# Performance work log

Measured on AMD Instinct MI355X. Metric: run time of the kernel, lower is better.

The kernel has to match this reference:

```python
import jax, jax.numpy as jnp
import numpy as np

# ---- static config (matches init_kwargs) ----
N_NODES = 100_000; N_GRAPHS = 100; NPG = 1000; GRID = 32  # ceil(sqrt(1000))
N_EDGES = 1_600_000
IN_DIM = 64; POS_DIM = 16; HID = 16; HEADS = 4; HD = HID * HEADS  # 64
OUT_DIM = 10; DIV_WEIGHT = 0.1; BN_EPS = 1e-5; NEG_SLOPE = 0.2


def _segment_softmax(e, dst, n):
    emax = jax.ops.segment_max(e, dst, num_segments=n)
    p = jnp.exp(e - emax[dst])
    denom = jax.ops.segment_sum(p, dst, num_segments=n)
    return p / (denom[dst] + 1e-16)


def _gat(x, src, dst, n, W, a_src, a_dst, extra=None):
    """GATv1-style conv: per-head linear, additive attention, segment softmax over dst."""
    H, D = a_src.shape
    h = (x @ W).reshape(n, H, D)          # [N,H,D]
    s = (h * a_src).sum(-1)               # [N,H]
    d = (h * a_dst).sum(-1)               # [N,H]
    e = s[src] + d[dst]
    if extra is not None:
        e = e + extra                     # positional attention bias [E,H]
    e = jax.nn.leaky_relu(e, NEG_SLOPE)
    alpha = _segment_softmax(e, dst, n)   # [E,H]
    out = jax.ops.segment_sum(alpha[:, :, None] * h[src], dst, num_segments=n)
    return out.reshape(n, H * D)


def _div_loss(W):
    # head-diversity / orthogonality regularizer on per-head weight slices
    in_dim = W.shape[0]
    Wh = W.reshape(in_dim, HEADS, HID).transpose(1, 0, 2).reshape(HEADS, -1)
    Wn = Wh / (jnp.linalg.norm(Wh, axis=-1, keepdims=True) + 1e-12)
    G = Wn @ Wn.T
    off = G - jnp.eye(HEADS, dtype=W.dtype)
    return DIV_WEIGHT * (off ** 2).sum() / (HEADS * (HEADS - 1))


def _grid_pos(n, dtype):
    # normalized grid positions per graph (equal-size graphs of NPG nodes)
    i = jnp.arange(n) % NPG
    return jnp.stack([(i // GRID) / (GRID - 1), (i % GRID) / (GRID - 1)], -1).astype(dtype)


def _forward(x, edge_index, batch,
             pe_W, pe_b,
             l0_pW, l0_pas, l0_pad, l0_posW, l0_posb, l0_dW, l0_das, l0_dad, l0_fW, l0_fb, l0_g, l0_b,
             l1_pW, l1_pas, l1_pad, l1_posW, l1_posb, l1_dW, l1_das, l1_dad, l1_fW, l1_fb, l1_g, l1_b,
             res_W, res_b, task_W, task_b):
    n = x.shape[0]
    src, dst = edge_index[0], edge_index[1]
    pos = _grid_pos(n, x.dtype)
    rel = pos[dst] - pos[src]             # [E,2]
    h = jnp.concatenate([x, pos @ pe_W + pe_b], -1)  # positional encoding concat [N,80]

    def layer(h_in, pW, pas, pad, posW, posb, dW, das, dad, fW, fb, g, b):
        pos_out = _gat(h_in, src, dst, n, pW, pas, pad, extra=rel @ posW + posb)
        div_out = _gat(h_in, src, dst, n, dW, das, dad)
        fused = jnp.concatenate([pos_out, div_out], -1) @ fW + fb
        mu = fused.mean(0)
        var = fused.var(0)
        bn = (fused - mu) / jnp.sqrt(var + BN_EPS) * g + b
        return jax.nn.elu(bn), _div_loss(dW)

    h1, dl0 = layer(h, l0_pW, l0_pas, l0_pad, l0_posW, l0_posb, l0_dW, l0_das, l0_dad, l0_fW, l0_fb, l0_g, l0_b)
    h2, dl1 = layer(h1, l1_pW, l1_pas, l1_pad, l1_posW, l1_posb, l1_dW, l1_das, l1_dad, l1_fW, l1_fb, l1_g, l1_b)
    h2 = h2 + (h1 @ res_W + res_b)        # residual on layer >0

    pooled = jax.ops.segment_sum(h2, batch, num_segments=N_GRAPHS) / NPG  # mean pool
    task = pooled @ task_W + task_b       # [N_GRAPHS, OUT_DIM]
    return task, dl0 + dl1


def setup_inputs() -> dict:
    key = jax.random.key(0)
    keys = iter(jax.random.split(key, 64))
    nk = lambda: next(keys)
    w = lambda shape: jax.random.normal(nk(), shape, jnp.float32) * 0.05
    x = jax.random.normal(nk(), (N_NODES, IN_DIM), jnp.float32)
    gid = jnp.repeat(jnp.arange(N_GRAPHS), N_EDGES // N_GRAPHS)
    src = gid * NPG + jax.random.randint(nk(), (N_EDGES,), 0, NPG)
    dst = gid * NPG + jax.random.randint(nk(), (N_EDGES,), 0, NPG)
    edge_index = jnp.stack([src, dst]).astype(jnp.int32)
    batch = jnp.repeat(jnp.arange(N_GRAPHS), NPG).astype(jnp.int32)
    IN0 = IN_DIM + POS_DIM
    inp = dict(x=x, edge_index=edge_index, batch=batch,
               pe_W=w((2, POS_DIM)), pe_b=jnp.zeros((POS_DIM,), jnp.float32))
    for pref, din in (('l0', IN0), ('l1', HD)):
        inp[pref + '_pW'] = w((din, HD)); inp[pref + '_pas'] = w((HEADS, HID)); inp[pref + '_pad'] = w((HEADS, HID))
        inp[pref + '_posW'] = w((2, HEADS)); inp[pref + '_posb'] = jnp.zeros((HEADS,), jnp.float32)
        inp[pref + '_dW'] = w((din, HD)); inp[pref + '_das'] = w((HEADS, HID)); inp[pref + '_dad'] = w((HEADS, HID))
        inp[pref + '_fW'] = w((2 * HD, HD)); inp[pref + '_fb'] = jnp.zeros((HD,), jnp.float32)
        inp[pref + '_g'] = jnp.ones((HD,), jnp.float32); inp[pref + '_b'] = jnp.zeros((HD,), jnp.float32)
    inp['res_W'] = w((HD, HD)); inp['res_b'] = jnp.zeros((HD,), jnp.float32)
    inp['task_W'] = w((HD, OUT_DIM)); inp['task_b'] = jnp.zeros((OUT_DIM,), jnp.float32)
    return inp


def reference(x, edge_index, batch,
              pe_W, pe_b,
              l0_pW, l0_pas, l0_pad, l0_posW, l0_posb, l0_dW, l0_das, l0_dad, l0_fW, l0_fb, l0_g, l0_b,
              l1_pW, l1_pas, l1_pad, l1_posW, l1_posb, l1_dW, l1_das, l1_dad, l1_fW, l1_fb, l1_g, l1_b,
              res_W, res_b, task_W, task_b):
    return _forward(x, edge_index, batch, pe_W, pe_b,
                    l0_pW, l0_pas, l0_pad, l0_posW, l0_posb, l0_dW, l0_das, l0_dad, l0_fW, l0_fb, l0_g, l0_b,
                    l1_pW, l1_pas, l1_pad, l1_posW, l1_posb, l1_dW, l1_das, l1_dad, l1_fW, l1_fb, l1_g, l1_b,
                    res_W, res_b, task_W, task_b)
```

## Files before the change

kernel.cpp:

```cpp
#include <hip/hip_runtime.h>
#include <math.h>

#define N_NODES   100000
#define N_GRAPHS  100
#define NPG       1000
#define N_EDGES   1600000
#define EPG       16000
#define HID       16
#define HEADS     4
#define HD        64
#define OUT_DIM   10
#define BN_EPS    1e-5f
#define NEG_SLOPE 0.2f

#define LDA 68
#define GG_BLOCKS 6250

static const size_t OFF_SPART = 0;
static const size_t OFF_PEWS  = 7000000;
static const size_t OFF_STAT1 = 7001000;
static const size_t OFF_WFRAG = 7010000;
static const size_t OFF_WF2   = 7020000;
static const size_t OFF_POOL  = 7100000;
static const size_t OFF_HL    = 8000000;
static const size_t OFF_F0    = 33600000;
static const size_t OFF_F1    = 40000000;
static const size_t OFF_SPSP  = 46400000;
static const size_t OFF_SPSD  = 46800000;
static const size_t OFF_DPD   = 47200000;
static const size_t OFF_STATS = 48000000;
static const size_t OFF_CSR   = 48000128;
static const size_t OFF_SRT   = 48100144;

__device__ inline unsigned bf_pack(float x, float y) {
    unsigned ux = __float_as_uint(x);
    unsigned uy = __float_as_uint(y);
    ux = (ux + 0x7FFFu + ((ux >> 16) & 1u)) >> 16;
    uy = ((uy + 0x7FFFu + ((uy >> 16) & 1u)) >> 16) << 16;
    return ux | uy;
}
__device__ inline float bf_lo(unsigned u) { return __uint_as_float(u << 16); }
__device__ inline float bf_hi(unsigned u) { return __uint_as_float(u & 0xFFFF0000u); }

typedef __attribute__((ext_vector_type(8))) short bf16x8;
typedef __attribute__((ext_vector_type(4))) float f32x4;

__device__ inline bf16x8 frag_from(unsigned a, unsigned b, unsigned c, unsigned d) {
    uint4 u{a, b, c, d};
    return *reinterpret_cast<bf16x8*>(&u);
}

__global__ __launch_bounds__(1024) void sort_edges(const int* __restrict__ ei,
                                                   int* __restrict__ csr_off,
                                                   int* __restrict__ sorted_src) {
    __shared__ int hist[1024];
    __shared__ int scan[1024];
    const int g = blockIdx.x;
    const int t = threadIdx.x;
    const int* src = ei;
    const int* dst = ei + N_EDGES;
    const int e0 = g * EPG;
    const int nbase = g * NPG;

    hist[t] = 0;
    __syncthreads();
    for (int i = t; i < EPG; i += 1024) {
        int d = dst[e0 + i] - nbase;
        atomicAdd(&hist[d], 1);
    }
    __syncthreads();
    scan[t] = hist[t];
    __syncthreads();
    for (int off = 1; off < 1024; off <<= 1) {
        int v = (t >= off) ? scan[t - off] : 0;
        __syncthreads();
        scan[t] += v;
        __syncthreads();
    }
    int excl = scan[t] - hist[t];
    if (t < NPG) csr_off[nbase + t] = e0 + excl;
    if (g == 0 && t == 0) csr_off[N_NODES] = N_EDGES;
    __syncthreads();
    hist[t] = excl;
    __syncthreads();
    for (int i = t; i < EPG; i += 1024) {
        int s = src[e0 + i];
        int d = dst[e0 + i] - nbase;
        int slot = atomicAdd(&hist[d], 1);
        sorted_src[e0 + slot] = s;
    }
}

__global__ __launch_bounds__(256) void prep_all(const float* __restrict__ peW, const float* __restrict__ peb,
                                                const float* __restrict__ pW0, const float* __restrict__ dW0,
                                                const float* __restrict__ pW1, const float* __restrict__ dW1,
                                                const float* __restrict__ fW0, const float* __restrict__ fW1,
                                                float* __restrict__ pe,
                                                uint4* __restrict__ wfA,
                                                uint4* __restrict__ wfD,
                                                float* __restrict__ pool2,
                                                float* __restrict__ stats0,
                                                float* __restrict__ stats1) {
    const int t = threadIdx.x;
    const int b = blockIdx.x;
    if (b == 0) {
        if (t < 128) {
            int r = t >> 6, c = t & 63;
            float sp = 0.f, sd = 0.f;
            for (int m = 0; m < 16; ++m) {
                sp += peW[r * 16 + m] * pW0[(64 + m) * 64 + c];
                sd += peW[r * 16 + m] * dW0[(64 + m) * 64 + c];
            }
            pe[r * 64 + c] = sp;
            pe[192 + r * 64 + c] = sd;
        } else if (t < 192) {
            int c = t & 63;
            float sp = 0.f, sd = 0.f;
            for (int m = 0; m < 16; ++m) {
                sp += peb[m] * pW0[(64 + m) * 64 + c];
                sd += peb[m] * dW0[(64 + m) * 64 + c];
            }
            pe[128 + c] = sp;
            pe[320 + c] = sd;
        }
    } else if (b == 1) {
        for (int i = t; i < 2 * 4 * 4 * 64; i += 256) {
            const int lane  = i & 63;
            const int ct    = (i >> 6) & 3;
            const int kk    = (i >> 8) & 3;
            const int layer = i >> 10;
            const float* W = layer ? fW1 : fW0;
            const int col = ct * 16 + (lane & 15);
            const int kb  = kk * 32 + (lane >> 4) * 8;
            uint4 u;
            u.x = bf_pack(W[(kb + 0) * 64 + col], W[(kb + 1) * 64 + col]);
            u.y = bf_pack(W[(kb + 2) * 64 + col], W[(kb + 3) * 64 + col]);
            u.z = bf_pack(W[(kb + 4) * 64 + col], W[(kb + 5) * 64 + col]);
            u.w = bf_pack(W[(kb + 6) * 64 + col], W[(kb + 7) * 64 + col]);
            wfA[i] = u;
        }
    } else if (b == 2) {
        for (int i = t; i < 2048; i += 256) {
            const int lane  = i & 63;
            const int ct    = (i >> 6) & 3;
            const int kk    = (i >> 8) & 1;
            const int mat   = (i >> 9) & 1;
            const int layer = i >> 10;
            const float* W = layer ? (mat ? dW1 : pW1) : (mat ? dW0 : pW0);
            const int col = ct * 16 + (lane & 15);
            const int kb  = kk * 32 + (lane >> 4) * 8;
            uint4 u;
            u.x = bf_pack(W[(kb + 0) * 64 + col], W[(kb + 1) * 64 + col]);
            u.y = bf_pack(W[(kb + 2) * 64 + col], W[(kb + 3) * 64 + col]);
            u.z = bf_pack(W[(kb + 4) * 64 + col], W[(kb + 5) * 64 + col]);
            u.w = bf_pack(W[(kb + 6) * 64 + col], W[(kb + 7) * 64 + col]);
            wfD[i] = u;
        }
    } else {
        for (int i = t; i < 2 * N_GRAPHS * 64; i += 256) pool2[i] = 0.f;
        if (t < 128) { stats0[t] = 0.f; stats1[t] = 0.f; }
    }
}

__global__ __launch_bounds__(128) void reduce_stats(const float* __restrict__ part,
                                                    float* __restrict__ stats, int nb) {
    const int c = threadIdx.x;
    const int per = (nb + gridDim.x - 1) / gridDim.x;
    const int b0 = blockIdx.x * per;
    int b1 = b0 + per; if (b1 > nb) b1 = nb;
    float s = 0.f;
    for (int b = b0; b < b1; ++b) s += part[(size_t)b * 128 + c];
    atomicAdd(&stats[c], s);
}

template <bool PE, bool BN>
__global__ __launch_bounds__(256) void gemm_dual_mfma(const float* __restrict__ A,
                                                      const unsigned* __restrict__ wf2,
                                                      const float* __restrict__ pe,
                                                      const float* __restrict__ pas,
                                                      const float* __restrict__ pad_,
                                                      const float* __restrict__ das,
                                                      const float* __restrict__ dad,
                                                      const float* __restrict__ posW,
                                                      const float* __restrict__ posb,
                                                      const float* __restrict__ stats,
                                                      const float* __restrict__ gamma,
                                                      const float* __restrict__ beta,
                                                      float* __restrict__ poolF,
                                                      unsigned* __restrict__ hl,
                                                      float* __restrict__ sps_p,
                                                      float* __restrict__ sps_d,
                                                      float2* __restrict__ dpd) {
    __shared__ float sD[4 * 2 * 16 * LDA];
    const int t = threadIdx.x;
    const int w = t >> 6, lane = t & 63;
    const int cidx = lane & 15, khi = lane >> 4;
    const int node0 = blockIdx.x * 64;

    bf16x8 wf[2][2][4];
#pragma unroll
    for (int mat = 0; mat < 2; ++mat)
#pragma unroll
        for (int kk = 0; kk < 2; ++kk)
#pragma unroll
            for (int ct = 0; ct < 4; ++ct)
                wf[mat][kk][ct] = *reinterpret_cast<const bf16x8*>(
                    wf2 + (size_t)((((mat * 2 + kk) * 4 + ct) * 64) + lane) * 4);

    const int node0w = node0 + w * 16;
    int gn = node0w + cidx; if (gn > N_NODES - 1) gn = N_NODES - 1;
    const float* ar = A + (size_t)gn * 64;
    bf16x8 ah[2], al[2];
#pragma unroll
    for (int kk = 0; kk < 2; ++kk) {
        const int k0 = kk * 32 + khi * 8;
        float4 f0 = *reinterpret_cast<const float4*>(ar + k0);
        float4 f1 = *reinterpret_cast<const float4*>(ar + k0 + 4);
        if (BN) {
            const float invN = 1.0f / (float)N_NODES;
            float4 sa = *reinterpret_cast<const float4*>(&stats[k0]);
            float4 sb = *reinterpret_cast<const float4*>(&stats[k0 + 4]);
            float4 qa = *reinterpret_cast<const float4*>(&stats[64 + k0]);
            float4 qb = *reinterpret_cast<const float4*>(&stats[64 + k0 + 4]);
            float4 ga = *reinterpret_cast<const float4*>(&gamma[k0]);
            float4 gb = *reinterpret_cast<const float4*>(&gamma[k0 + 4]);
            float4 ba = *reinterpret_cast<const float4*>(&beta[k0]);
            float4 bb = *reinterpret_cast<const float4*>(&beta[k0 + 4]);
            float sc[8], sh[8];
            float ss[8] = {sa.x, sa.y, sa.z, sa.w, sb.x, sb.y, sb.z, sb.w};
            float qq[8] = {qa.x, qa.y, qa.z, qa.w, qb.x, qb.y, qb.z, qb.w};
            float gg[8] = {ga.x, ga.y, ga.z, ga.w, gb.x, gb.y, gb.z, gb.w};
            float bt[8] = {ba.x, ba.y, ba.z, ba.w, bb.x, bb.y, bb.z, bb.w};
#pragma unroll
            for (int i = 0; i < 8; ++i) {
                float mu = ss[i] * invN;
                float var = qq[i] * invN - mu * mu;
                float iv = rsqrtf(var + BN_EPS);
                sc[i] = iv * gg[i];
                sh[i] = bt[i] - mu * sc[i];
            }
            auto ap = [&](float v, int i) {
                float r = fmaf(v, sc[i], sh[i]);
                return r > 0.f ? r : (__expf(r) - 1.f);
            };
            f0.x = ap(f0.x, 0); f0.y = ap(f0.y, 1); f0.z = ap(f0.z, 2); f0.w = ap(f0.w, 3);
            f1.x = ap(f1.x, 4); f1.y = ap(f1.y, 5); f1.z = ap(f1.z, 6); f1.w = ap(f1.w, 7);
            if (node0w < N_NODES) {
                const int node_l = node0w + cidx;
                const bool okn = node_l < N_NODES;
                const int gl = node_l / NPG;
                const int g0 = node0w / NPG;
                int lastn = node0w + 15; if (lastn > N_NODES - 1) lastn = N_NODES - 1;
                const int g1 = lastn / NPG;
                float p8[8] = {f0.x, f0.y, f0.z, f0.w, f1.x, f1.y, f1.z, f1.w};
                {
                    const bool m = okn && (gl == g0);
#pragma unroll
                    for (int i = 0; i < 8; ++i) {
                        float tv = m ? p8[i] : 0.f;
                        tv += __shfl_xor(tv, 1); tv += __shfl_xor(tv, 2);
                        tv += __shfl_xor(tv, 4); tv += __shfl_xor(tv, 8);
                        if (cidx == 0) atomicAdd(&poolF[g0 * 64 + k0 + i], tv);
                    }
                }
                if (g1 != g0) {
                    const bool m = okn && (gl == g1);
#pragma unroll
                    for (int i = 0; i < 8; ++i) {
                        float tv = m ? p8[i] : 0.f;
                        tv += __shfl_xor(tv, 1); tv += __shfl_xor(tv, 2);
                        tv += __shfl_xor(tv, 4); tv += __shfl_xor(tv, 8);
                        if (cidx == 0) atomicAdd(&poolF[g1 * 64 + k0 + i], tv);
                    }
                }
            }
        }
        unsigned h0 = bf_pack(f0.x, f0.y), h1 = bf_pack(f0.z, f0.w);
        unsigned h2 = bf_pack(f1.x, f1.y), h3 = bf_pack(f1.z, f1.w);
        unsigned l0 = bf_pack(f0.x - bf_lo(h0), f0.y - bf_hi(h0));
        unsigned l1 = bf_pack(f0.z - bf_lo(h1), f0.w - bf_hi(h1));
        unsigned l2 = bf_pack(f1.x - bf_lo(h2), f1.y - bf_hi(h2));
        unsigned l3 = bf_pack(f1.z - bf_lo(h3), f1.w - bf_hi(h3));
        ah[kk] = frag_from(h0, h1, h2, h3);
        al[kk] = frag_from(l0, l1, l2, l3);
    }

    f32x4 ap4[4], ad4[4];
#pragma unroll
    for (int ct = 0; ct < 4; ++ct) { ap4[ct] = 0.f; ad4[ct] = 0.f; }
#pragma unroll
    for (int ct = 0; ct < 4; ++ct) {
        ap4[ct] = __builtin_amdgcn_mfma_f32_16x16x32_bf16(ah[0], wf[0][0][ct], ap4[ct], 0, 0, 0);
        ap4[ct] = __builtin_amdgcn_mfma_f32_16x16x32_bf16(ah[1], wf[0][1][ct], ap4[ct], 0, 0, 0);
        ap4[ct] = __builtin_amdgcn_mfma_f32_16x16x32_bf16(al[0], wf[0][0][ct], ap4[ct], 0, 0, 0);
        ap4[ct] = __builtin_amdgcn_mfma_f32_16x16x32_bf16(al[1], wf[0][1][ct], ap4[ct], 0, 0, 0);
        ad4[ct] = __builtin_amdgcn_mfma_f32_16x16x32_bf16(ah[0], wf[1][0][ct], ad4[ct], 0, 0, 0);
        ad4[ct] = __builtin_amdgcn_mfma_f32_16x16x32_bf16(ah[1], wf[1][1][ct], ad4[ct], 0, 0, 0);
        ad4[ct] = __builtin_amdgcn_mfma_f32_16x16x32_bf16(al[0], wf[1][0][ct], ad4[ct], 0, 0, 0);
        ad4[ct] = __builtin_amdgcn_mfma_f32_16x16x32_bf16(al[1], wf[1][1][ct], ad4[ct], 0, 0, 0);
    }

    {
        float* base = sD + w * (2 * 16 * LDA);
#pragma unroll
        for (int ct = 0; ct < 4; ++ct)
#pragma unroll
            for (int q = 0; q < 4; ++q) {
                base[(khi * 4 + q) * LDA + ct * 16 + cidx]                 = ap4[ct][q];
                base[16 * LDA + (khi * 4 + q) * LDA + ct * 16 + cidx]      = ad4[ct][q];
            }
    }
    __syncthreads();

    const int tx = t & 15, ty = t >> 4;
    const int c4 = tx * 4;
    float4 accp[4], accd[4];
#pragma unroll
    for (int j = 0; j < 4; ++j) {
        const int n = ty * 4 + j;
        const float* bp = sD + (n >> 4) * (2 * 16 * LDA) + (n & 15) * LDA;
        accp[j] = *reinterpret_cast<const float4*>(bp + c4);
        accd[j] = *reinterpret_cast<const float4*>(bp + 16 * LDA + c4);
    }

    if (PE) {
        float4 pp0 = *reinterpret_cast<const float4*>(&pe[c4]);
        float4 pp1 = *reinterpret_cast<const float4*>(&pe[64 + c4]);
        float4 ppb = *reinterpret_cast<const float4*>(&pe[128 + c4]);
        float4 pd0 = *reinterpret_cast<const float4*>(&pe[192 + c4]);
        float4 pd1 = *reinterpret_cast<const float4*>(&pe[256 + c4]);
        float4 pdb = *reinterpret_cast<const float4*>(&pe[320 + c4]);
#pragma unroll
        for (int j = 0; j < 4; ++j) {
            int node = node0 + ty * 4 + j;
            int r = node % NPG;
            float px = (float)(r >> 5) * (1.0f / 31.0f);
            float py = (float)(r & 31) * (1.0f / 31.0f);
            accp[j].x += px * pp0.x + py * pp1.x + ppb.x;
            accp[j].y += px * pp0.y + py * pp1.y + ppb.y;
            accp[j].z += px * pp0.z + py * pp1.z + ppb.z;
            accp[j].w += px * pp0.w + py * pp1.w + ppb.w;
            accd[j].x += px * pd0.x + py * pd1.x + pdb.x;
            accd[j].y += px * pd0.y + py * pd1.y + pdb.y;
            accd[j].z += px * pd0.z + py * pd1.z + pdb.z;
            accd[j].w += px * pd0.w + py * pd1.w + pdb.w;
        }
    }

    float4 pasv = *reinterpret_cast<const float4*>(&pas[c4]);
    float4 padv = *reinterpret_cast<const float4*>(&pad_[c4]);
    float4 dasv = *reinterpret_cast<const float4*>(&das[c4]);
    float4 dadv = *reinterpret_cast<const float4*>(&dad[c4]);
    const int h = tx >> 2;
    const float pw0 = posW[h], pw1 = posW[4 + h], pb = posb[h];
    const int cu = tx * 2;
#pragma unroll
    for (int j = 0; j < 4; ++j) {
        const int node = node0 + ty * 4 + j;
        float vps = accp[j].x * pasv.x + accp[j].y * pasv.y + accp[j].z * pasv.z + accp[j].w * pasv.w;
        float vpd = accp[j].x * padv.x + accp[j].y * padv.y + accp[j].z * padv.z + accp[j].w * padv.w;
        float vds = accd[j].x * dasv.x + accd[j].y * dasv.y + accd[j].z * dasv.z + accd[j].w * dasv.w;
        float vdd = accd[j].x * dadv.x + accd[j].y * dadv.y + accd[j].z * dadv.z + accd[j].w * dadv.w;
        vps += __shfl_xor(vps, 1); vps += __shfl_xor(vps, 2);
        vpd += __shfl_xor(vpd, 1); vpd += __shfl_xor(vpd, 2);
        vds += __shfl_xor(vds, 1); vds += __shfl_xor(vds, 2);
        vdd += __shfl_xor(vdd, 1); vdd += __shfl_xor(vdd, 2);
        if (node < N_NODES) {
            uint2 up, ud;
            up.x = bf_pack(accp[j].x, accp[j].y); up.y = bf_pack(accp[j].z, accp[j].w);
            ud.x = bf_pack(accd[j].x, accd[j].y); ud.y = bf_pack(accd[j].z, accd[j].w);
            *reinterpret_cast<uint2*>(&hl[(size_t)node * 64 + cu])      = up;
            *reinterpret_cast<uint2*>(&hl[(size_t)node * 64 + 32 + cu]) = ud;
            if ((tx & 3) == 0) {
                const int r = node % NPG;
                const float pxn = (float)(r >> 5) * (1.0f / 31.0f);
                const float pyn = (float)(r & 31) * (1.0f / 31.0f);
                const float posdot = pxn * pw0 + pyn * pw1;
                sps_p[node * 4 + h] = vps - posdot;
                sps_d[node * 4 + h] = vds;
                dpd[node * 4 + h] = float2{vpd + posdot + pb, vdd};
            }
        }
    }
}

__global__ __launch_bounds__(256) void gat_gemm(const unsigned* __restrict__ hl,
                                                const float* __restrict__ sps_p,
                                                const float* __restrict__ sps_d,
                                                const float2* __restrict__ dpd,
                                                const int* __restrict__ csr_off,
                                                const int* __restrict__ sorted_src,
                                                const unsigned* __restrict__ wfrag,
                                                const float* __restrict__ bias,
                                                float* __restrict__ outF,
                                                float* __restrict__ spart) {
    __shared__ unsigned sCat[16 * LDA];
    const int t = threadIdx.x;
    const int w = t >> 6, lane = t & 63;

    const int orig = blockIdx.x;
    const int xcd = orig & 7;
    const int qq = GG_BLOCKS >> 3, rr = GG_BLOCKS & 7;
    const int lb = (xcd < rr ? xcd * (qq + 1) : rr * (qq + 1) + (xcd - rr) * qq) + (orig >> 3);
    const int node0 = lb * 16;

    const int j1 = lane >> 3;
    const int p1 = (lane >> 2) & 1;
    const int h1 = lane & 3;
    const int phneed = ((lane >> 5) << 2) | ((lane & 31) >> 3);
    const float* __restrict__ spl = p1 ? sps_d : sps_p;

    for (int i = 0; i < 4; ++i) {
        const int v = node0 + w * 4 + i;
        const float2 dv1 = dpd[(size_t)v * 4 + h1];
        const float dval1 = p1 ? dv1.y : dv1.x;
        const int beg = __builtin_amdgcn_readfirstlane(csr_off[v]);
        const int end = __builtin_amdgcn_readfirstlane(csr_off[v + 1]);

        float2 acc = {0.f, 0.f};
        float wpart = 0.f;
        int e = beg;
        const int nfull = (end - beg) >> 3;

        int sA = 0, sB = 0;
        float svA = 0.f, svB = 0.f;
        if (nfull >= 1) { sA = sorted_src[e + j1]; svA = spl[(size_t)sA * 4 + h1]; }
        if (nfull >= 2) { sB = sorted_src[e + 8 + j1]; }

        for (int k = 0; k < nfull; ++k, e += 8) {
            int sC = 0;
            if (k + 2 < nfull) sC = sorted_src[e + 16 + j1];
            if (k + 1 < nfull) svB = spl[(size_t)sB * 4 + h1];
            float elog = svA + dval1;
            elog = fmaxf(elog, NEG_SLOPE * elog);
            float wv = __expf(elog);
            wpart += wv;
#pragma unroll
            for (int jj = 0; jj < 8; ++jj) {
                int sj = __builtin_amdgcn_readlane(sA, jj * 8);
                float wj = __shfl(wv, jj * 8 + phneed);
                unsigned u = hl[((size_t)sj << 6) + lane];
                acc.x = fmaf(wj, bf_lo(u), acc.x);
                acc.y = fmaf(wj, bf_hi(u), acc.y);
            }
            sA = sB; sB = sC; svA = svB;
        }

        if (e < end) {
            const int nj = end - e;
            int ee = e + j1; if (ee >= end) ee = end - 1;
            int s = sorted_src[ee];
            float sval = spl[(size_t)s * 4 + h1];
            float elog = sval + dval1;
            elog = fmaxf(elog, NEG_SLOPE * elog);
            float wv = __expf(elog);
            if (j1 >= nj) wv = 0.f;
            wpart += wv;
            for (int jj = 0; jj < nj; ++jj) {
                int sj = __builtin_amdgcn_readlane(s, jj * 8);
                float wj = __shfl(wv, jj * 8 + phneed);
                unsigned u = hl[((size_t)sj << 6) + lane];
                acc.x = fmaf(wj, bf_lo(u), acc.x);
                acc.y = fmaf(wj, bf_hi(u), acc.y);
            }
        }
        wpart += __shfl_xor(wpart, 8);
        wpart += __shfl_xor(wpart, 16);
        wpart += __shfl_xor(wpart, 32);
        const float wsum = __shfl(wpart, phneed);
        const float inv = 1.0f / (wsum + 1e-16f);
        sCat[(w * 4 + i) * LDA + lane] = bf_pack(acc.x * inv, acc.y * inv);
    }
    __syncthreads();

    const int cidx = lane & 15, khi = lane >> 4;
    bf16x8 wfr[4];
#pragma unroll
    for (int kk = 0; kk < 4; ++kk)
        wfr[kk] = *reinterpret_cast<const bf16x8*>(wfrag + (size_t)((kk * 4 + w) * 64 + lane) * 4);
    const float biasv = bias[w * 16 + cidx];

    f32x4 acc4 = 0.f;
#pragma unroll
    for (int kk = 0; kk < 4; ++kk) {
        bf16x8 a = *reinterpret_cast<const bf16x8*>(&sCat[cidx * LDA + kk * 16 + khi * 4]);
        acc4 = __builtin_amdgcn_mfma_f32_16x16x32_bf16(a, wfr[kk], acc4, 0, 0, 0);
    }

    float ls = 0.f, lq = 0.f;
#pragma unroll
    for (int q = 0; q < 4; ++q) {
        float v = acc4[q] + biasv;
        outF[(size_t)(node0 + khi * 4 + q) * 64 + w * 16 + cidx] = v;
        ls += v;
        lq = fmaf(v, v, lq);
    }
    ls += __shfl_xor(ls, 16); ls += __shfl_xor(ls, 32);
    lq += __shfl_xor(lq, 16); lq += __shfl_xor(lq, 32);
    if (khi == 0) {
        spart[(size_t)lb * 128 + w * 16 + cidx]      = ls;
        spart[(size_t)lb * 128 + 64 + w * 16 + cidx] = lq;
    }
}

template <bool WRITEF>
__global__ __launch_bounds__(256) void bn_elu(float* __restrict__ F, const float* __restrict__ stats,
                                              const float* __restrict__ gamma, const float* __restrict__ beta,
                                              float* __restrict__ pooled) {
    __shared__ float red[256];
    const int t = threadIdx.x;
    const int idx = blockIdx.x * 256 + t;
    const int c = t & 63;
    float mu = stats[c] * (1.0f / (float)N_NODES);
    float var = stats[64 + c] * (1.0f / (float)N_NODES) - mu * mu;
    float inv = rsqrtf(var + BN_EPS);
    float v = (F[idx] - mu) * inv * gamma[c] + beta[c];
    v = (v > 0.f) ? v : expm1f(v);
    if (WRITEF) F[idx] = v;
    red[t] = v;
    __syncthreads();
    if (t < 64) {
        float s = red[c] + red[64 + c] + red[128 + c] + red[192 + c];
        int g = (blockIdx.x * 4) / NPG;
        atomicAdd(&pooled[g * 64 + c], s);
    }
}

__global__ __launch_bounds__(64) void task_head(const float* __restrict__ pooled,
                                                const float* __restrict__ pooledF0,
                                                const float* __restrict__ resW,
                                                const float* __restrict__ resb,
                                                const float* __restrict__ taskW,
                                                const float* __restrict__ taskb,
                                                float* __restrict__ out) {
    const int g = blockIdx.x;
    const int c = threadIdx.x;
    float rc = 0.f;
    const float* pf = pooledF0 + g * 64;
    for (int k = 0; k < 64; ++k)
        rc = fmaf(pf[k], resW[k * 64 + c], rc);
    float p = (pooled[g * 64 + c] + rc) * (1.0f / (float)NPG) + resb[c];
#pragma unroll
    for (int o = 0; o < OUT_DIM; ++o) {
        float partial = p * taskW[c * OUT_DIM + o];
#pragma unroll
        for (int m = 1; m < 64; m <<= 1) partial += __shfl_xor(partial, m);
        if (c == 0) out[g * OUT_DIM + o] = partial + taskb[o];
    }
}

__global__ __launch_bounds__(256) void div_loss(const float* __restrict__ dW0,
                                                const float* __restrict__ dW1,
                                                float* __restrict__ out) {
    __shared__ float red[16][16];
    float total = 0.f;
    for (int layer = 0; layer < 2; ++layer) {
        const float* W = layer ? dW1 : dW0;
        const int din = layer ? 64 : 80;
        const int p = threadIdx.x & 15;
        const int s16 = threadIdx.x >> 4;
        const int i = p >> 2, j = p & 3;
        float acc = 0.f;
        const int Kk = din * 16;
        for (int kk = s16; kk < Kk; kk += 16) {
            int rrow = kk >> 4, cc = kk & 15;
            acc += W[rrow * 64 + i * 16 + cc] * W[rrow * 64 + j * 16 + cc];
        }
        red[p][s16] = acc;
        __syncthreads();
        if (threadIdx.x < 16) {
            float s = 0.f;
            for (int m = 0; m < 16; ++m) s += red[threadIdx.x][m];
            red[threadIdx.x][0] = s;
        }
        __syncthreads();
        if (threadIdx.x == 0) {
            float G[4][4], nrm[4];
            for (int a = 0; a < 4; ++a)
                for (int b = 0; b < 4; ++b) G[a][b] = red[a * 4 + b][0];
            for (int a = 0; a < 4; ++a) nrm[a] = sqrtf(G[a][a]) + 1e-12f;
            float l = 0.f;
            for (int a = 0; a < 4; ++a)
                for (int b = 0; b < 4; ++b) {
                    float gn = G[a][b] / (nrm[a] * nrm[b]);
                    float off = gn - (a == b ? 1.f : 0.f);
                    l += off * off;
                }
            total += 0.1f * l / 12.f;
        }
        __syncthreads();
    }
    if (threadIdx.x == 0) *out = total;
}

extern "C" void kernel_launch(void* const* d_in, const int* in_sizes, int n_in,
                              void* d_out, int out_size, void* d_ws, size_t ws_size,
                              hipStream_t stream) {
    const float* x      = (const float*)d_in[0];
    const int*   ei     = (const int*)d_in[1];
    const float* peW    = (const float*)d_in[3];
    const float* peb    = (const float*)d_in[4];

    const float* l_pW[2]   = {(const float*)d_in[5],  (const float*)d_in[17]};
    const float* l_pas[2]  = {(const float*)d_in[6],  (const float*)d_in[18]};
    const float* l_pad[2]  = {(const float*)d_in[7],  (const float*)d_in[19]};
    const float* l_posW[2] = {(const float*)d_in[8],  (const float*)d_in[20]};
    const float* l_posb[2] = {(const float*)d_in[9],  (const float*)d_in[21]};
    const float* l_dW[2]   = {(const float*)d_in[10], (const float*)d_in[22]};
    const float* l_das[2]  = {(const float*)d_in[11], (const float*)d_in[23]};
    const float* l_dad[2]  = {(const float*)d_in[12], (const float*)d_in[24]};
    const float* l_fW[2]   = {(const float*)d_in[13], (const float*)d_in[25]};
    const float* l_fb[2]   = {(const float*)d_in[14], (const float*)d_in[26]};
    const float* l_g[2]    = {(const float*)d_in[15], (const float*)d_in[27]};
    const float* l_b[2]    = {(const float*)d_in[16], (const float*)d_in[28]};
    const float* res_W  = (const float*)d_in[29];
    const float* res_b  = (const float*)d_in[30];
    const float* task_W = (const float*)d_in[31];
    const float* task_b = (const float*)d_in[32];

    float* ws = (float*)d_ws;
    float* spart   = ws + OFF_SPART;
    float* pe_ws   = ws + OFF_PEWS;
    float* stats1  = ws + OFF_STAT1;
    float* wfrag   = ws + OFF_WFRAG;
    float* wfrag2  = ws + OFF_WF2;
    float* pooled  = ws + OFF_POOL;
    float* pooledF0= ws + OFF_POOL + 6400;
    unsigned* hl   = (unsigned*)(ws + OFF_HL);
    float* F0      = ws + OFF_F0;
    float* F1      = ws + OFF_F1;
    float* sps_p   = ws + OFF_SPSP;
    float* sps_d   = ws + OFF_SPSD;
    float2* dpd    = (float2*)(ws + OFF_DPD);
    float* stats0  = ws + OFF_STATS;
    int*   csr_off    = (int*)(ws + OFF_CSR);
    int*   sorted_src = (int*)(ws + OFF_SRT);
    float* out = (float*)d_out;

    const int GEMM_BLOCKS = (N_NODES + 63) / 64;
    const int BN_BLOCKS   = N_NODES * 64 / 256;

    sort_edges<<<N_GRAPHS, 1024, 0, stream>>>(ei, csr_off, sorted_src);
    prep_all<<<4, 256, 0, stream>>>(peW, peb, l_pW[0], l_dW[0], l_pW[1], l_dW[1],
                                    l_fW[0], l_fW[1], pe_ws,
                                    (uint4*)wfrag, (uint4*)wfrag2,
                                    pooled, stats0, stats1);

    gemm_dual_mfma<true, false><<<GEMM_BLOCKS, 256, 0, stream>>>(x, (const unsigned*)wfrag2, pe_ws,
        l_pas[0], l_pad[0], l_das[0], l_dad[0], l_posW[0], l_posb[0],
        stats0, l_g[0], l_b[0], pooledF0,
        hl, sps_p, sps_d, dpd);
    gat_gemm<<<GG_BLOCKS, 256, 0, stream>>>(hl, sps_p, sps_d, dpd, csr_off, sorted_src,
        (const unsigned*)wfrag, l_fb[0], F0, spart);
    reduce_stats<<<32, 128, 0, stream>>>(spart, stats0, GG_BLOCKS);

    gemm_dual_mfma<false, true><<<GEMM_BLOCKS, 256, 0, stream>>>(F0, (const unsigned*)wfrag2 + 4096, pe_ws,
        l_pas[1], l_pad[1], l_das[1], l_dad[1], l_posW[1], l_posb[1],
        stats0, l_g[0], l_b[0], pooledF0,
        hl, sps_p, sps_d, dpd);
    gat_gemm<<<GG_BLOCKS, 256, 0, stream>>>(hl, sps_p, sps_d, dpd, csr_off, sorted_src,
        (const unsigned*)wfrag + 4096, l_fb[1], F1, spart);
    reduce_stats<<<32, 128, 0, stream>>>(spart, stats1, GG_BLOCKS);
    bn_elu<false><<<BN_BLOCKS, 256, 0, stream>>>(F1, stats1, l_g[1], l_b[1], pooled);

    task_head<<<N_GRAPHS, 64, 0, stream>>>(pooled, pooledF0, res_W, res_b,
                                           task_W, task_b, out);
    div_loss<<<1, 256, 0, stream>>>(l_dW[0], l_dW[1], out + 1000);
}
```

Before: 501.1 us.

## Merge sort and prep kernels, batch gather loads, coarsen final BN-pool

Folds the weight-prep kernel into the edge-sort launch as extra blocks, which removes one kernel launch. Rewrites the gather inner loop so all eight neighbor row loads are issued before any FMA, aiming for more memory-level parallelism. Replaces the per-element bn_elu with a pool_bn kernel where each block handles 200 nodes. This cuts the block count and the pooled atomics sharply, at the cost of far fewer blocks in flight.

```diff
diff --git a/kernel.cpp b/kernel.cpp
--- a/kernel.cpp
+++ b/kernel.cpp
@@ -15,6 +15,8 @@
 
 #define LDA 68
 #define GG_BLOCKS 6250
+#define PB_PER_GRAPH 5
+#define PB_NODES 200
 
 static const size_t OFF_SPART = 0;
 static const size_t OFF_PEWS  = 7000000;
@@ -50,13 +52,87 @@
     return *reinterpret_cast<bf16x8*>(&u);
 }
 
-__global__ __launch_bounds__(1024) void sort_edges(const int* __restrict__ ei,
-                                                   int* __restrict__ csr_off,
-                                                   int* __restrict__ sorted_src) {
+__global__ __launch_bounds__(1024) void sort_prep(const int* __restrict__ ei,
+                                                  int* __restrict__ csr_off,
+                                                  int* __restrict__ sorted_src,
+                                                  const float* __restrict__ peW, const float* __restrict__ peb,
+                                                  const float* __restrict__ pW0, const float* __restrict__ dW0,
+                                                  const float* __restrict__ pW1, const float* __restrict__ dW1,
+                                                  const float* __restrict__ fW0, const float* __restrict__ fW1,
+                                                  float* __restrict__ pe,
+                                                  uint4* __restrict__ wfA,
+                                                  uint4* __restrict__ wfD,
+                                                  float* __restrict__ pool2,
+                                                  float* __restrict__ stats0,
+                                                  float* __restrict__ stats1) {
+    const int g = blockIdx.x;
+    const int t = threadIdx.x;
+    if (g >= N_GRAPHS) {
+        const int b = g - N_GRAPHS;
+        if (b == 0) {
+            if (t < 128) {
+                int r = t >> 6, c = t & 63;
+                float sp = 0.f, sd = 0.f;
+                for (int m = 0; m < 16; ++m) {
+                    sp += peW[r * 16 + m] * pW0[(64 + m) * 64 + c];
+                    sd += peW[r * 16 + m] * dW0[(64 + m) * 64 + c];
+                }
+                pe[r * 64 + c] = sp;
+                pe[192 + r * 64 + c] = sd;
+            } else if (t < 192) {
+                int c = t & 63;
+                float sp = 0.f, sd = 0.f;
+                for (int m = 0; m < 16; ++m) {
+                    sp += peb[m] * pW0[(64 + m) * 64 + c];
+                    sd += peb[m] * dW0[(64 + m) * 64 + c];
+                }
+                pe[128 + c] = sp;
+                pe[320 + c] = sd;
+            }
+        } else if (b == 1) {
+            if (t < 256)
+            for (int i = t; i < 2 * 4 * 4 * 64; i += 256) {
+                const int lane  = i & 63;
+                const int ct    = (i >> 6) & 3;
+                const int kk    = (i >> 8) & 3;
+                const int layer = i >> 10;
+                const float* W = layer ? fW1 : fW0;
+                const int col = ct * 16 + (lane & 15);
+                const int kb  = kk * 32 + (lane >> 4) * 8;
+                uint4 u;
+                u.x = bf_pack(W[(kb + 0) * 64 + col], W[(kb + 1) * 64 + col]);
+                u.y = bf_pack(W[(kb + 2) * 64 + col], W[(kb + 3) * 64 + col]);
+                u.z = bf_pack(W[(kb + 4) * 64 + col], W[(kb + 5) * 64 + col]);
+                u.w = bf_pack(W[(kb + 6) * 64 + col], W[(kb + 7) * 64 + col]);
+                wfA[i] = u;
+            }
+        } else if (b == 2) {
+            if (t < 256)
+            for (int i = t; i < 2048; i += 256) {
+                const int lane  = i & 63;
+                const int ct    = (i >> 6) & 3;
+                const int kk    = (i >> 8) & 1;
+                const int mat   = (i >> 9) & 1;
+                const int layer = i >> 10;
+                const float* W = layer ? (mat ? dW1 : pW1) : (mat ? dW0 : pW0);
+                const int col = ct * 16 + (lane & 15);
+                const int kb  = kk * 32 + (lane >> 4) * 8;
+                uint4 u;
+                u.x = bf_pack(W[(kb + 0) * 64 + col], W[(kb + 1) * 64 + col]);
+                u.y = bf_pack(W[(kb + 2) * 64 + col], W[(kb + 3) * 64 + col]);
+                u.z = bf_pack(W[(kb + 4) * 64 + col], W[(kb + 5) * 64 + col]);
+                u.w = bf_pack(W[(kb + 6) * 64 + col], W[(kb + 7) * 64 + col]);
+                wfD[i] = u;
+            }
+        } else {
+            for (int i = t; i < 2 * N_GRAPHS * 64; i += 1024) pool2[i] = 0.f;
+            if (t < 128) { stats0[t] = 0.f; stats1[t] = 0.f; }
+        }
+        return;
+    }
+
     __shared__ int hist[1024];
     __shared__ int scan[1024];
-    const int g = blockIdx.x;
-    const int t = threadIdx.x;
     const int* src = ei;
     const int* dst = ei + N_EDGES;
     const int e0 = g * EPG;
@@ -88,77 +164,6 @@
         int d = dst[e0 + i] - nbase;
         int slot = atomicAdd(&hist[d], 1);
         sorted_src[e0 + slot] = s;
-    }
-}
-
-__global__ __launch_bounds__(256) void prep_all(const float* __restrict__ peW, const float* __restrict__ peb,
-                                                const float* __restrict__ pW0, const float* __restrict__ dW0,
-                                                const float* __restrict__ pW1, const float* __restrict__ dW1,
-                                                const float* __restrict__ fW0, const float* __restrict__ fW1,
-                                                float* __restrict__ pe,
-                                                uint4* __restrict__ wfA,
-                                                uint4* __restrict__ wfD,
-                                                float* __restrict__ pool2,
-                                                float* __restrict__ stats0,
-                                                float* __restrict__ stats1) {
-    const int t = threadIdx.x;
-    const int b = blockIdx.x;
-    if (b == 0) {
-        if (t < 128) {
-            int r = t >> 6, c = t & 63;
-            float sp = 0.f, sd = 0.f;
-            for (int m = 0; m < 16; ++m) {
-                sp += peW[r * 16 + m] * pW0[(64 + m) * 64 + c];
-                sd += peW[r * 16 + m] * dW0[(64 + m) * 64 + c];
-            }
-            pe[r * 64 + c] = sp;
-            pe[192 + r * 64 + c] = sd;
-        } else if (t < 192) {
-            int c = t & 63;
-            float sp = 0.f, sd = 0.f;
-            for (int m = 0; m < 16; ++m) {
-                sp += peb[m] * pW0[(64 + m) * 64 + c];
-                sd += peb[m] * dW0[(64 + m) * 64 + c];
-            }
-            pe[128 + c] = sp;
-            pe[320 + c] = sd;
-        }
-    } else if (b == 1) {
-        for (int i = t; i < 2 * 4 * 4 * 64; i += 256) {
-            const int lane  = i & 63;
-            const int ct    = (i >> 6) & 3;
-            const int kk    = (i >> 8) & 3;
-            const int layer = i >> 10;
-            const float* W = layer ? fW1 : fW0;
-            const int col = ct * 16 + (lane & 15);
-            const int kb  = kk * 32 + (lane >> 4) * 8;
-            uint4 u;
-            u.x = bf_pack(W[(kb + 0) * 64 + col], W[(kb + 1) * 64 + col]);
-            u.y = bf_pack(W[(kb + 2) * 64 + col], W[(kb + 3) * 64 + col]);
-            u.z = bf_pack(W[(kb + 4) * 64 + col], W[(kb + 5) * 64 + col]);
-            u.w = bf_pack(W[(kb + 6) * 64 + col], W[(kb + 7) * 64 + col]);
-            wfA[i] = u;
-        }
-    } else if (b == 2) {
-        for (int i = t; i < 2048; i += 256) {
-            const int lane  = i & 63;
-            const int ct    = (i >> 6) & 3;
-            const int kk    = (i >> 8) & 1;
-            const int mat   = (i >> 9) & 1;
-            const int layer = i >> 10;
-            const float* W = layer ? (mat ? dW1 : pW1) : (mat ? dW0 : pW0);
-            const int col = ct * 16 + (lane & 15);
-            const int kb  = kk * 32 + (lane >> 4) * 8;
-            uint4 u;
-            u.x = bf_pack(W[(kb + 0) * 64 + col], W[(kb + 1) * 64 + col]);
-            u.y = bf_pack(W[(kb + 2) * 64 + col], W[(kb + 3) * 64 + col]);
-            u.z = bf_pack(W[(kb + 4) * 64 + col], W[(kb + 5) * 64 + col]);
-            u.w = bf_pack(W[(kb + 6) * 64 + col], W[(kb + 7) * 64 + col]);
-            wfD[i] = u;
-        }
-    } else {
-        for (int i = t; i < 2 * N_GRAPHS * 64; i += 256) pool2[i] = 0.f;
-        if (t < 128) { stats0[t] = 0.f; stats1[t] = 0.f; }
     }
 }
 
@@ -435,14 +440,38 @@
             elog = fmaxf(elog, NEG_SLOPE * elog);
             float wv = __expf(elog);
             wpart += wv;
-#pragma unroll
-            for (int jj = 0; jj < 8; ++jj) {
-                int sj = __builtin_amdgcn_readlane(sA, jj * 8);
-                float wj = __shfl(wv, jj * 8 + phneed);
-                unsigned u = hl[((size_t)sj << 6) + lane];
-                acc.x = fmaf(wj, bf_lo(u), acc.x);
-                acc.y = fmaf(wj, bf_hi(u), acc.y);
-            }
+            int sj0 = __builtin_amdgcn_readlane(sA, 0);
+            int sj1 = __builtin_amdgcn_readlane(sA, 8);
+            int sj2 = __builtin_amdgcn_readlane(sA, 16);
+            int sj3 = __builtin_amdgcn_readlane(sA, 24);
+            int sj4 = __builtin_amdgcn_readlane(sA, 32);
+            int sj5 = __builtin_amdgcn_readlane(sA, 40);
+            int sj6 = __builtin_amdgcn_readlane(sA, 48);
+            int sj7 = __builtin_amdgcn_readlane(sA, 56);
+            float wj0 = __shfl(wv, 0 + phneed);
+            float wj1 = __shfl(wv, 8 + phneed);
+            float wj2 = __shfl(wv, 16 + phneed);
+            float wj3 = __shfl(wv, 24 + phneed);
+            float wj4 = __shfl(wv, 32 + phneed);
+            float wj5 = __shfl(wv, 40 + phneed);
+            float wj6 = __shfl(wv, 48 + phneed);
+            float wj7 = __shfl(wv, 56 + phneed);
+            unsigned u0 = hl[((size_t)sj0 << 6) + lane];
+            unsigned u1 = hl[((size_t)sj1 << 6) + lane];
+            unsigned u2 = hl[((size_t)sj2 << 6) + lane];
+            unsigned u3 = hl[((size_t)sj3 << 6) + lane];
+            unsigned u4 = hl[((size_t)sj4 << 6) + lane];
+            unsigned u5 = hl[((size_t)sj5 << 6) + lane];
+            unsigned u6 = hl[((size_t)sj6 << 6) + lane];
+            unsigned u7 = hl[((size_t)sj7 << 6) + lane];
+            acc.x = fmaf(wj0, bf_lo(u0), acc.x); acc.y = fmaf(wj0, bf_hi(u0), acc.y);
+            acc.x = fmaf(wj1, bf_lo(u1), acc.x); acc.y = fmaf(wj1, bf_hi(u1), acc.y);
+            acc.x = fmaf(wj2, bf_lo(u2), acc.x); acc.y = fmaf(wj2, bf_hi(u2), acc.y);
+            acc.x = fmaf(wj3, bf_lo(u3), acc.x); acc.y = fmaf(wj3, bf_hi(u3), acc.y);
+            acc.x = fmaf(wj4, bf_lo(u4), acc.x); acc.y = fmaf(wj4, bf_hi(u4), acc.y);
+            acc.x = fmaf(wj5, bf_lo(u5), acc.x); acc.y = fmaf(wj5, bf_hi(u5), acc.y);
+            acc.x = fmaf(wj6, bf_lo(u6), acc.x); acc.y = fmaf(wj6, bf_hi(u6), acc.y);
+            acc.x = fmaf(wj7, bf_lo(u7), acc.x); acc.y = fmaf(wj7, bf_hi(u7), acc.y);
             sA = sB; sB = sC; svA = svB;
         }
 
@@ -503,27 +532,30 @@
     }
 }
 
-template <bool WRITEF>
-__global__ __launch_bounds__(256) void bn_elu(float* __restrict__ F, const float* __restrict__ stats,
-                                              const float* __restrict__ gamma, const float* __restrict__ beta,
-                                              float* __restrict__ pooled) {
+__global__ __launch_bounds__(256) void pool_bn(const float* __restrict__ F, const float* __restrict__ stats,
+                                               const float* __restrict__ gamma, const float* __restrict__ beta,
+                                               float* __restrict__ pooled) {
     __shared__ float red[256];
+    const int b = blockIdx.x;
+    const int g = b / PB_PER_GRAPH;
+    const int n0 = g * NPG + (b % PB_PER_GRAPH) * PB_NODES;
     const int t = threadIdx.x;
-    const int idx = blockIdx.x * 256 + t;
-    const int c = t & 63;
-    float mu = stats[c] * (1.0f / (float)N_NODES);
-    float var = stats[64 + c] * (1.0f / (float)N_NODES) - mu * mu;
-    float inv = rsqrtf(var + BN_EPS);
-    float v = (F[idx] - mu) * inv * gamma[c] + beta[c];
-    v = (v > 0.f) ? v : expm1f(v);
-    if (WRITEF) F[idx] = v;
-    red[t] = v;
-    __syncthreads();
-    if (t < 64) {
-        float s = red[c] + red[64 + c] + red[128 + c] + red[192 + c];
-        int g = (blockIdx.x * 4) / NPG;
-        atomicAdd(&pooled[g * 64 + c], s);
-    }
+    const int c = t & 63, rg = t >> 6;
+    const float mu = stats[c] * (1.0f / (float)N_NODES);
+    const float var = stats[64 + c] * (1.0f / (float)N_NODES) - mu * mu;
+    const float iv = rsqrtf(var + BN_EPS);
+    const float sc = iv * gamma[c];
+    const float sh = beta[c] - mu * sc;
+    float s = 0.f;
+    for (int i = rg; i < PB_NODES; i += 4) {
+        float v = fmaf(F[(size_t)(n0 + i) * 64 + c], sc, sh);
+        v = (v > 0.f) ? v : expm1f(v);
+        s += v;
+    }
+    red[t] = s;
+    __syncthreads();
+    if (t < 64)
+        atomicAdd(&pooled[g * 64 + c], red[c] + red[64 + c] + red[128 + c] + red[192 + c]);
 }
 
 __global__ __launch_bounds__(64) void task_head(const float* __restrict__ pooled,
@@ -638,13 +670,11 @@
     float* out = (float*)d_out;
 
     const int GEMM_BLOCKS = (N_NODES + 63) / 64;
-    const int BN_BLOCKS   = N_NODES * 64 / 256;
-
-    sort_edges<<<N_GRAPHS, 1024, 0, stream>>>(ei, csr_off, sorted_src);
-    prep_all<<<4, 256, 0, stream>>>(peW, peb, l_pW[0], l_dW[0], l_pW[1], l_dW[1],
-                                    l_fW[0], l_fW[1], pe_ws,
-                                    (uint4*)wfrag, (uint4*)wfrag2,
-                                    pooled, stats0, stats1);
+    const int PB_BLOCKS   = N_GRAPHS * PB_PER_GRAPH;
+
+    sort_prep<<<N_GRAPHS + 4, 1024, 0, stream>>>(ei, csr_off, sorted_src,
+        peW, peb, l_pW[0], l_dW[0], l_pW[1], l_dW[1], l_fW[0], l_fW[1],
+        pe_ws, (uint4*)wfrag, (uint4*)wfrag2, pooled, stats0, stats1);
 
     gemm_dual_mfma<true, false><<<GEMM_BLOCKS, 256, 0, stream>>>(x, (const unsigned*)wfrag2, pe_ws,
         l_pas[0], l_pad[0], l_das[0], l_dad[0], l_posW[0], l_posb[0],
@@ -661,7 +691,7 @@
     gat_gemm<<<GG_BLOCKS, 256, 0, stream>>>(hl, sps_p, sps_d, dpd, csr_off, sorted_src,
         (const unsigned*)wfrag + 4096, l_fb[1], F1, spart);
     reduce_stats<<<32, 128, 0, stream>>>(spart, stats1, GG_BLOCKS);
-    bn_elu<false><<<BN_BLOCKS, 256, 0, stream>>>(F1, stats1, l_g[1], l_b[1], pooled);
+    pool_bn<<<PB_BLOCKS, 256, 0, stream>>>(F1, stats1, l_g[1], l_b[1], pooled);
 
     task_head<<<N_GRAPHS, 64, 0, stream>>>(pooled, pooledF0, res_W, res_b,
                                            task_W, task_b, out);
```

Measured after the change: 498.7 us. About the same (-0.5%).
